# Kernel optimization log

Hardware: AMD Instinct MI355X
Metric: run time of the kernel (lower is better)

Reference implementation:

```python
import jax, jax.numpy as jnp
import numpy as np

N = 100000
E = 1600000


def seg_softmax(alpha, dst, n):
    # numerically stable softmax over variable-size destination segments
    amax = jax.ops.segment_max(alpha, dst, num_segments=n)
    amax = jnp.where(jnp.isfinite(amax), amax, 0.0)
    ex = jnp.exp(alpha - amax[dst])
    denom = jax.ops.segment_sum(ex, dst, num_segments=n)
    return ex / (denom[dst] + 1e-16)


def setup_inputs() -> dict:
    key = jax.random.key(0)
    ks = jax.random.split(key, 24)
    p = lambda k, shape: (jax.random.normal(k, shape, jnp.float32) * 0.1)
    x = jax.random.normal(ks[0], (N, 3), jnp.float32)
    edge_index = jax.random.randint(ks[1], (2, E), 0, N, dtype=jnp.int64)
    return {
        'x': x, 'edge_index': edge_index,
        # GATConv(3,16,heads=4): shared lin (no bias), att_src/att_dst, final bias
        'W1': p(ks[2], (3, 64)), 'att_src1': p(ks[3], (4, 16)), 'att_dst1': p(ks[4], (4, 16)), 'b1': jnp.zeros((64,), jnp.float32),
        # GATv2Conv(64,16,heads=2): lin_l, lin_r (both with bias), att, final bias
        'W2l': p(ks[5], (64, 32)), 'b2l': jnp.zeros((32,), jnp.float32),
        'W2r': p(ks[6], (64, 32)), 'b2r': jnp.zeros((32,), jnp.float32),
        'att2': p(ks[7], (2, 16)), 'b2': jnp.zeros((32,), jnp.float32),
        # TransformerConv(32,7,heads=1): q/k/v lins + skip lin (all with bias)
        'Wq': p(ks[8], (32, 7)), 'bq': jnp.zeros((7,), jnp.float32),
        'Wk': p(ks[9], (32, 7)), 'bk': jnp.zeros((7,), jnp.float32),
        'Wv': p(ks[10], (32, 7)), 'bv': jnp.zeros((7,), jnp.float32),
        'Wskip': p(ks[11], (32, 7)), 'bskip': jnp.zeros((7,), jnp.float32),
    }


def reference(x, edge_index, W1, att_src1, att_dst1, b1, W2l, b2l, W2r, b2r, att2, b2,
              Wq, bq, Wk, bk, Wv, bv, Wskip, bskip):
    n = x.shape[0]
    loop = jnp.arange(n, dtype=edge_index.dtype)
    # edge index with self-loops (GATConv / GATv2Conv default add_self_loops=True)
    src = jnp.concatenate([edge_index[0], loop])
    dst = jnp.concatenate([edge_index[1], loop])

    # ---- layer 1: GATConv(3, 16, heads=4) ----
    h = (x @ W1).reshape(n, 4, 16)                       # [N,H,C]
    a_src = (h * att_src1[None]).sum(-1)                 # [N,H]
    a_dst = (h * att_dst1[None]).sum(-1)
    alpha = jax.nn.leaky_relu(a_src[src] + a_dst[dst], 0.2)  # [E+N,H]
    alpha = seg_softmax(alpha, dst, n)
    out = jax.ops.segment_sum(h[src] * alpha[..., None], dst, num_segments=n)
    x1 = jax.nn.relu(out.reshape(n, 64) + b1)

    # ---- layer 2: GATv2Conv(64, 16, heads=2) ----
    hl = (x1 @ W2l + b2l).reshape(n, 2, 16)
    hr = (x1 @ W2r + b2r).reshape(n, 2, 16)
    e = jax.nn.leaky_relu(hl[src] + hr[dst], 0.2)        # [E+N,H,C]
    alpha = (e * att2[None]).sum(-1)                     # [E+N,H]
    alpha = seg_softmax(alpha, dst, n)
    out = jax.ops.segment_sum(hl[src] * alpha[..., None], dst, num_segments=n)
    x2 = out.reshape(n, 32) + b2

    # ---- layer 3: TransformerConv(32, 7, heads=1); no self-loops by default ----
    s, d = edge_index[0], edge_index[1]
    q = x2 @ Wq + bq                                     # [N,7] (H=1,C=7)
    k = x2 @ Wk + bk
    v = x2 @ Wv + bv
    scale = 1.0 / jnp.sqrt(jnp.float32(7.0))
    alpha = (q[d] * k[s]).sum(-1) * scale                # [E]
    alpha = seg_softmax(alpha, d, n)
    out = jax.ops.segment_sum(v[s] * alpha[:, None], d, num_segments=n)
    x3 = out + (x2 @ Wskip + bskip)                      # root_weight skip connection
    return x3
```

## Files before the change

kernel.cpp:

```cpp
#include <hip/hip_runtime.h>
#include <hip/hip_bf16.h>

typedef __hip_bfloat16 bf16;

static __device__ __forceinline__ float us2f(unsigned short u) {
    union { unsigned int i; float f; } c; c.i = ((unsigned int)u) << 16; return c.f;
}
static __device__ __forceinline__ unsigned short f2us(float f) {
    union { float f; unsigned int i; } c; c.f = f;
    unsigned int r = c.i + 0x7FFF + ((c.i >> 16) & 1);
    return (unsigned short)(r >> 16);
}

static __device__ __forceinline__ int probe_isf32(const unsigned short* xr, int* sflag) {
    int tid = threadIdx.x;
    if (tid < 64) {
        int bad = 0;
        for (int i = tid; i < 1024; i += 64) {
            int ex = (xr[2 * i] >> 7) & 0xFF;
            if (ex < 110 || ex > 135) bad++;
        }
#pragma unroll
        for (int m = 32; m >= 1; m >>= 1) bad += __shfl_xor(bad, m);
        if (tid == 0) *sflag = (bad > 256) ? 1 : 0;
    }
    __syncthreads();
    return *sflag;
}

static __device__ __forceinline__ int ld_edge(const int* er, size_t i, int idx64) {
    return idx64 ? er[2 * i] : er[i];
}


struct CvtArgs { const void* p[19]; int sz[19]; };

static __device__ __forceinline__ float cvt_elem(const void* p, int off, int isf32) {
    return isf32 ? ((const float*)p)[off] : __bfloat162float(((const bf16*)p)[off]);
}

__global__ __launch_bounds__(256) void k_convert(CvtArgs a, float* __restrict__ dst, int total,
                                                 int nbconv, float* __restrict__ Wcat,
                                                 float* __restrict__ bcat, int* __restrict__ bcur) {
    __shared__ int sflag;
    int isf32 = probe_isf32((const unsigned short*)a.p[0], &sflag);
    int tid = threadIdx.x;
    if ((int)blockIdx.x == nbconv) {
#pragma unroll
        for (int t4 = 0; t4 < 4; ++t4) {
            int idx = t4 * 256 + tid;
            int c = idx & 31, g = c >> 3, cc = c & 7, kk = idx >> 5;
            const void* Wg = (g == 0) ? a.p[11] : (g == 1) ? a.p[17] : (g == 2) ? a.p[13] : a.p[15];
            Wcat[idx] = (cc < 7) ? cvt_elem(Wg, kk * 7 + cc, isf32) : 0.f;
        }
        if (tid < 32) {
            int g = tid >> 3, cc = tid & 7;
            const void* Bg = (g == 0) ? a.p[12] : (g == 1) ? a.p[18] : (g == 2) ? a.p[14] : a.p[16];
            bcat[tid] = (cc < 7) ? cvt_elem(Bg, cc, isf32) : 0.f;
        }
        bcur[tid] = 0;
        return;
    }
    int t = blockIdx.x * 256 + tid;
    if (t >= total) return;
    int base = 0, seg = -1, off = 0;
#pragma unroll
    for (int i = 0; i < 19; i++) {
        if (seg < 0 && t < base + a.sz[i]) { seg = i; off = t - base; }
        base += a.sz[i];
    }
    dst[t] = cvt_elem(a.p[seg], off, isf32);
}


__global__ __launch_bounds__(1024) void k_bscatter(const int* __restrict__ er,
                                                   int* __restrict__ bcur, int* __restrict__ bkt,
                                                   int E, int NB, int C) {
    __shared__ int cnt[256];
    __shared__ int res[256];
    __shared__ int sflag;
    int tid = threadIdx.x;
    if (tid < 64) {
        int lim = (E < 1024) ? E : 1024;
        int nz = 0;
        for (int i = tid; i < lim; i += 64) if (er[2 * i + 1] != 0) nz++;
#pragma unroll
        for (int m = 32; m >= 1; m >>= 1) nz += __shfl_xor(nz, m);
        if (tid == 0) sflag = (nz < ((E < 1024 ? E : 1024) >> 1)) ? 1 : 0;
    }
    if (tid < 256) cnt[tid] = 0;
    __syncthreads();
    int idx64 = sflag;
    int base = blockIdx.x * 4096 + tid;
    int pk[4], bv[4];
    bool val[4];
#pragma unroll
    for (int k = 0; k < 4; ++k) {
        int e = base + k * 1024;
        val[k] = (e < E);
        if (val[k]) {
            int s = ld_edge(er, (size_t)e, idx64);
            int d = ld_edge(er, (size_t)E + e, idx64);
            bv[k] = d >> 10;
            pk[k] = (s << 10) | (d & 1023);
            atomicAdd(&cnt[bv[k]], 1);
        }
    }
    __syncthreads();
    if (tid < NB) {
        int c = cnt[tid];
        res[tid] = c ? atomicAdd(&bcur[tid], c) : 0;
        cnt[tid] = 0;
    }
    __syncthreads();
#pragma unroll
    for (int k = 0; k < 4; ++k) {
        if (val[k]) {
            int r = res[bv[k]] + atomicAdd(&cnt[bv[k]], 1);
            if (r < C) bkt[(size_t)bv[k] * C + r] = pk[k];
        }
    }
}

__global__ __launch_bounds__(1024) void k_bbuild(const int* __restrict__ bkt, const int* __restrict__ bcur,
                                                 int2* __restrict__ off2, int* __restrict__ csr, int N, int C) {
    __shared__ int sm[1024];
    int b = blockIdx.x, tid = threadIdx.x;
    size_t base = (size_t)b * C;
    int m = bcur[b]; if (m > C) m = C;
    sm[tid] = 0;
    __syncthreads();
    const int* bp = bkt + base;
    for (int i = tid; i < m; i += 1024) atomicAdd(&sm[bp[i] & 1023], 1);
    __syncthreads();
    int v = sm[tid];
    for (int d = 1; d < 1024; d <<= 1) {
        int t = (tid >= d) ? sm[tid - d] : 0;
        __syncthreads();
        sm[tid] += t;
        __syncthreads();
    }
    int excl = sm[tid] - v;
    int node = (b << 10) + tid;
    if (node < N) off2[node] = make_int2((int)base + excl, (int)base + excl + v);
    __syncthreads();
    sm[tid] = excl;
    __syncthreads();
    for (int i = tid; i < m; i += 1024) {
        int p = bp[i];
        int r = atomicAdd(&sm[p & 1023], 1);
        csr[base + r] = p >> 10;
    }
}


__global__ __launch_bounds__(256) void k_l1_transform(const float* __restrict__ x, const float* __restrict__ W1,
                                                      const float* __restrict__ att_s, const float* __restrict__ att_d,
                                                      float4* __restrict__ x4, float* __restrict__ as1,
                                                      float* __restrict__ ad1, int N) {
    int tid = threadIdx.x;
    int node = blockIdx.x * 4 + (tid >> 6);
    if (node >= N) return;
    int lane = tid & 63;
    float x0 = x[node * 3 + 0];
    float x1 = x[node * 3 + 1];
    float x2 = x[node * 3 + 2];
    float h = x0 * W1[lane] + x1 * W1[64 + lane] + x2 * W1[128 + lane];
    if (lane == 0) x4[node] = make_float4(x0, x1, x2, 0.f);
    float ts = h * att_s[lane];
    float td = h * att_d[lane];
    for (int m = 8; m >= 1; m >>= 1) { ts += __shfl_xor(ts, m); td += __shfl_xor(td, m); }
    if ((lane & 15) == 0) {
        as1[node * 4 + (lane >> 4)] = ts;
        ad1[node * 4 + (lane >> 4)] = td;
    }
}

__global__ __launch_bounds__(256) void k_l1_agg(const float4* __restrict__ x4, const float4* __restrict__ as4,
                                                const float4* __restrict__ ad4p, const int2* __restrict__ off2,
                                                const int* __restrict__ csr, const float* __restrict__ W1,
                                                const float* __restrict__ b1,
                                                float* __restrict__ x1, int N) {
    int tid = threadIdx.x;
    int node = blockIdx.x * 16 + (tid >> 4);
    if (node >= N) return;
    int sl = tid & 15;
    int lane = tid & 63;
    int lb = lane & 48;

    float4 ad = ad4p[node];
    int2 ee = off2[node];
    int e0 = ee.x, e1 = ee.y;

    float v[16];
#pragma unroll
    for (int i = 0; i < 16; ++i) v[i] = 0.f;

    for (int jj = e0 + sl; jj < e1; jj += 16) {
        int s = csr[jj];
        float4 a = as4[s];
        float4 xv = x4[s];
        float z0 = a.x + ad.x, z1 = a.y + ad.y, z2 = a.z + ad.z, z3 = a.w + ad.w;
        z0 = (z0 > 0.f) ? z0 : 0.2f * z0;
        z1 = (z1 > 0.f) ? z1 : 0.2f * z1;
        z2 = (z2 > 0.f) ? z2 : 0.2f * z2;
        z3 = (z3 > 0.f) ? z3 : 0.2f * z3;
        float w0 = __expf(z0), w1 = __expf(z1), w2 = __expf(z2), w3 = __expf(z3);
        v[0] += w0 * xv.x; v[1] += w0 * xv.y; v[2]  += w0 * xv.z; v[3]  += w0;
        v[4] += w1 * xv.x; v[5] += w1 * xv.y; v[6]  += w1 * xv.z; v[7]  += w1;
        v[8] += w2 * xv.x; v[9] += w2 * xv.y; v[10] += w2 * xv.z; v[11] += w2;
        v[12] += w3 * xv.x; v[13] += w3 * xv.y; v[14] += w3 * xv.z; v[15] += w3;
    }

#pragma unroll
    for (int d = 8; d >= 1; d >>= 1) {
#pragma unroll
        for (int i = 0; i < 16; ++i) {
            if (i < d) {
                float a = v[i], b = v[i + d];
                float send = (sl & d) ? a : b;
                float recv = __shfl_xor(send, d);
                v[i] = ((sl & d) ? b : a) + recv;
            }
        }
    }
    float r = v[0];

    float agx[4], agy[4], agz[4], dn[4];
#pragma unroll
    for (int h = 0; h < 4; ++h) {
        agx[h] = __shfl(r, lb + 4 * h + 0);
        agy[h] = __shfl(r, lb + 4 * h + 1);
        agz[h] = __shfl(r, lb + 4 * h + 2);
        dn[h]  = __shfl(r, lb + 4 * h + 3);
    }

    {
        float4 a = as4[node];
        float4 xv = x4[node];
        float z0 = a.x + ad.x, z1 = a.y + ad.y, z2 = a.z + ad.z, z3 = a.w + ad.w;
        z0 = (z0 > 0.f) ? z0 : 0.2f * z0;
        z1 = (z1 > 0.f) ? z1 : 0.2f * z1;
        z2 = (z2 > 0.f) ? z2 : 0.2f * z2;
        z3 = (z3 > 0.f) ? z3 : 0.2f * z3;
        float w0 = __expf(z0), w1 = __expf(z1), w2 = __expf(z2), w3 = __expf(z3);
        agx[0] += w0 * xv.x; agy[0] += w0 * xv.y; agz[0] += w0 * xv.z; dn[0] += w0;
        agx[1] += w1 * xv.x; agy[1] += w1 * xv.y; agz[1] += w1 * xv.z; dn[1] += w1;
        agx[2] += w2 * xv.x; agy[2] += w2 * xv.y; agz[2] += w2 * xv.z; dn[2] += w2;
        agx[3] += w3 * xv.x; agy[3] += w3 * xv.y; agz[3] += w3 * xv.z; dn[3] += w3;
    }

#pragma unroll
    for (int h = 0; h < 4; ++h) {
        int j = h * 16 + sl;
        float inv = 1.f / (dn[h] + 1e-16f);
        float o = (agx[h] * W1[j] + agy[h] * W1[64 + j] + agz[h] * W1[128 + j]) * inv + b1[j];
        x1[(size_t)node * 64 + j] = (o > 0.f) ? o : 0.f;
    }
}


__global__ __launch_bounds__(256) void k_l2_transform(const float* __restrict__ x1,
                                                      const float* __restrict__ W2l, const float* __restrict__ b2l,
                                                      const float* __restrict__ W2r, const float* __restrict__ b2r,
                                                      unsigned short* __restrict__ hlb, float* __restrict__ hr, int N) {
    __shared__ float xs[64 * 68];
    int t = threadIdx.x;
    int node0 = blockIdx.x * 64;
    int nrem = N - node0; if (nrem > 64) nrem = 64;
    const float4* xg = (const float4*)x1;
#pragma unroll
    for (int it = 0; it < 4; ++it) {
        int id = it * 256 + t;
        int row = id >> 4, c4 = id & 15;
        float4 v = make_float4(0.f, 0.f, 0.f, 0.f);
        if (row < nrem) v = xg[(size_t)(node0 + row) * 16 + c4];
        *(float4*)&xs[row * 68 + c4 * 4] = v;
    }
    __syncthreads();
    int nt = t >> 4;
    int jt = t & 15;
    int jq = jt & 7;
    int jc = jq * 4;
    const float4* W4 = (const float4*)((jt < 8) ? W2l : W2r);
    const float4* B4 = (const float4*)((jt < 8) ? b2l : b2r);
    float4 bb = B4[jq];
    float4 acc[4];
#pragma unroll
    for (int i = 0; i < 4; ++i) acc[i] = bb;
#pragma unroll 2
    for (int k4 = 0; k4 < 16; ++k4) {
        float4 w0 = W4[(k4 * 4 + 0) * 8 + jq];
        float4 w1 = W4[(k4 * 4 + 1) * 8 + jq];
        float4 w2 = W4[(k4 * 4 + 2) * 8 + jq];
        float4 w3 = W4[(k4 * 4 + 3) * 8 + jq];
#pragma unroll
        for (int i = 0; i < 4; ++i) {
            float4 xv = *(const float4*)&xs[(nt + i * 16) * 68 + k4 * 4];
            acc[i].x += xv.x * w0.x + xv.y * w1.x + xv.z * w2.x + xv.w * w3.x;
            acc[i].y += xv.x * w0.y + xv.y * w1.y + xv.z * w2.y + xv.w * w3.y;
            acc[i].z += xv.x * w0.z + xv.y * w1.z + xv.z * w2.z + xv.w * w3.z;
            acc[i].w += xv.x * w0.w + xv.y * w1.w + xv.z * w2.w + xv.w * w3.w;
        }
    }
#pragma unroll
    for (int i = 0; i < 4; ++i) {
        int row = nt + i * 16;
        if (row < nrem) {
            size_t node = node0 + row;
            if (jt < 8) {
                uint2 p;
                p.x = (unsigned)f2us(acc[i].x) | ((unsigned)f2us(acc[i].y) << 16);
                p.y = (unsigned)f2us(acc[i].z) | ((unsigned)f2us(acc[i].w) << 16);
                *(uint2*)&hlb[node * 32 + jc] = p;
            } else {
                *(float4*)&hr[node * 32 + jc] = acc[i];
            }
        }
    }
}

__global__ __launch_bounds__(256) void k_l2_agg(const unsigned short* __restrict__ hlb, const float* __restrict__ hr,
                                                const float* __restrict__ att2, const float* __restrict__ b2,
                                                const int2* __restrict__ off2, const int* __restrict__ csr,
                                                float* __restrict__ x2, int N) {
    int tid = threadIdx.x;
    int node = blockIdx.x * 16 + (tid >> 4);
    if (node >= N) return;
    int sl = tid & 15;

    float hrd[32];
    {
        const float4* hr4 = (const float4*)(hr + (size_t)node * 32);
#pragma unroll
        for (int q = 0; q < 8; ++q) {
            float4 v = hr4[q];
            hrd[4 * q + 0] = v.x; hrd[4 * q + 1] = v.y;
            hrd[4 * q + 2] = v.z; hrd[4 * q + 3] = v.w;
        }
    }

    float accA[16], accB[16];
#pragma unroll
    for (int i = 0; i < 16; ++i) { accA[i] = 0.f; accB[i] = 0.f; }
    float den0 = 0.f, den1 = 0.f;

    int2 ee = off2[node];
    int e0 = ee.x, e1 = ee.y;
    for (int jj = e0 + sl; jj < e1; jj += 16) {
        int s = csr[jj];
        const uint4* hp = (const uint4*)(hlb + (size_t)s * 32);
        uint4 u0 = hp[0], u1 = hp[1], u2 = hp[2], u3 = hp[3];
        unsigned int uu[16] = {u0.x, u0.y, u0.z, u0.w, u1.x, u1.y, u1.z, u1.w,
                               u2.x, u2.y, u2.z, u2.w, u3.x, u3.y, u3.z, u3.w};
        float t0 = 0.f, t1 = 0.f;
#pragma unroll
        for (int q = 0; q < 8; ++q) {
            float lo = __uint_as_float(uu[q] << 16);
            float hi = __uint_as_float(uu[q] & 0xFFFF0000u);
            float el = lo + hrd[2 * q];     el = fmaxf(el, 0.2f * el);
            float eh = hi + hrd[2 * q + 1]; eh = fmaxf(eh, 0.2f * eh);
            t0 += att2[2 * q] * el + att2[2 * q + 1] * eh;
        }
#pragma unroll
        for (int q = 8; q < 16; ++q) {
            float lo = __uint_as_float(uu[q] << 16);
            float hi = __uint_as_float(uu[q] & 0xFFFF0000u);
            float el = lo + hrd[2 * q];     el = fmaxf(el, 0.2f * el);
            float eh = hi + hrd[2 * q + 1]; eh = fmaxf(eh, 0.2f * eh);
            t1 += att2[2 * q] * el + att2[2 * q + 1] * eh;
        }
        float w0 = __expf(t0), w1 = __expf(t1);
        den0 += w0; den1 += w1;
#pragma unroll
        for (int q = 0; q < 8; ++q) {
            accA[2 * q]     += w0 * __uint_as_float(uu[q] << 16);
            accA[2 * q + 1] += w0 * __uint_as_float(uu[q] & 0xFFFF0000u);
        }
#pragma unroll
        for (int q = 8; q < 16; ++q) {
            accB[2 * (q - 8)]     += w1 * __uint_as_float(uu[q] << 16);
            accB[2 * (q - 8) + 1] += w1 * __uint_as_float(uu[q] & 0xFFFF0000u);
        }
    }

#pragma unroll
    for (int d = 8; d >= 1; d >>= 1) {
#pragma unroll
        for (int i = 0; i < 16; ++i) {
            if (i < d) {
                { float a = accA[i], b = accA[i + d];
                  float send = (sl & d) ? a : b;
                  float recv = __shfl_xor(send, d);
                  accA[i] = ((sl & d) ? b : a) + recv; }
                { float a = accB[i], b = accB[i + d];
                  float send = (sl & d) ? a : b;
                  float recv = __shfl_xor(send, d);
                  accB[i] = ((sl & d) ? b : a) + recv; }
            }
        }
        den0 += __shfl_xor(den0, d);
        den1 += __shfl_xor(den1, d);
    }
    float sumA = accA[0];
    float sumB = accB[0];

    float hr0 = hr[(size_t)node * 32 + sl];
    float hr1 = hr[(size_t)node * 32 + 16 + sl];
    float hl0 = us2f(hlb[(size_t)node * 32 + sl]);
    float hl1 = us2f(hlb[(size_t)node * 32 + 16 + sl]);
    float ea = hl0 + hr0; ea = fmaxf(ea, 0.2f * ea);
    float eb = hl1 + hr1; eb = fmaxf(eb, 0.2f * eb);
    float p0 = att2[sl] * ea;
    float p1 = att2[16 + sl] * eb;
    p0 += __shfl_xor(p0, 1); p0 += __shfl_xor(p0, 2); p0 += __shfl_xor(p0, 4); p0 += __shfl_xor(p0, 8);
    p1 += __shfl_xor(p1, 1); p1 += __shfl_xor(p1, 2); p1 += __shfl_xor(p1, 4); p1 += __shfl_xor(p1, 8);
    float w0 = __expf(p0), w1 = __expf(p1);
    sumA += w0 * hl0; den0 += w0;
    sumB += w1 * hl1; den1 += w1;

    x2[(size_t)node * 32 + sl]      = sumA / (den0 + 1e-16f) + b2[sl];
    x2[(size_t)node * 32 + 16 + sl] = sumB / (den1 + 1e-16f) + b2[16 + sl];
}


__global__ __launch_bounds__(256) void k_l3_transform(const float* __restrict__ x2,
                                                      const float4* __restrict__ Wc4, const float4* __restrict__ bc4,
                                                      float* __restrict__ QS, unsigned short* __restrict__ KVb, int N) {
    __shared__ float xs[128 * 36];
    int t = threadIdx.x;
    int node0 = blockIdx.x * 128;
    int nrem = N - node0; if (nrem > 128) nrem = 128;
    const float4* xg = (const float4*)x2;
#pragma unroll
    for (int it = 0; it < 4; ++it) {
        int id = it * 256 + t;
        int row = id >> 3, c4 = id & 7;
        float4 v = make_float4(0.f, 0.f, 0.f, 0.f);
        if (row < nrem) v = xg[(size_t)(node0 + row) * 8 + c4];
        *(float4*)&xs[row * 36 + c4 * 4] = v;
    }
    __syncthreads();
    int nt = t >> 3;
    int jt = t & 7;
    float4 bb = bc4[jt];
    float4 acc[4];
#pragma unroll
    for (int i = 0; i < 4; ++i) acc[i] = bb;
#pragma unroll 2
    for (int k4 = 0; k4 < 8; ++k4) {
        float4 w0 = Wc4[(k4 * 4 + 0) * 8 + jt];
        float4 w1 = Wc4[(k4 * 4 + 1) * 8 + jt];
        float4 w2 = Wc4[(k4 * 4 + 2) * 8 + jt];
        float4 w3 = Wc4[(k4 * 4 + 3) * 8 + jt];
#pragma unroll
        for (int i = 0; i < 4; ++i) {
            float4 xv = *(const float4*)&xs[(nt + i * 32) * 36 + k4 * 4];
            acc[i].x += xv.x * w0.x + xv.y * w1.x + xv.z * w2.x + xv.w * w3.x;
            acc[i].y += xv.x * w0.y + xv.y * w1.y + xv.z * w2.y + xv.w * w3.y;
            acc[i].z += xv.x * w0.z + xv.y * w1.z + xv.z * w2.z + xv.w * w3.z;
            acc[i].w += xv.x * w0.w + xv.y * w1.w + xv.z * w2.w + xv.w * w3.w;
        }
    }
#pragma unroll
    for (int i = 0; i < 4; ++i) {
        int row = nt + i * 32;
        if (row < nrem) {
            size_t node = node0 + row;
            if (jt < 4) {
                *(float4*)(QS + node * 16 + jt * 4) = acc[i];
            } else {
                uint2 p;
                p.x = (unsigned)f2us(acc[i].x) | ((unsigned)f2us(acc[i].y) << 16);
                p.y = (unsigned)f2us(acc[i].z) | ((unsigned)f2us(acc[i].w) << 16);
                *(uint2*)&KVb[node * 16 + (size_t)(jt - 4) * 4] = p;
            }
        }
    }
}

__global__ __launch_bounds__(256) void k_l3_agg(const float* __restrict__ QS, const unsigned short* __restrict__ KVb,
                                                const int2* __restrict__ off2, const int* __restrict__ csr,
                                                float* __restrict__ out, int N) {
    int tid = threadIdx.x;
    int node = blockIdx.x * 32 + (tid >> 3);
    if (node >= N) return;
    int sl = tid & 7;
    int lane = tid & 63;
    const float scale = 0.3779644730092272f;
    const float4* q4 = (const float4*)(QS + (size_t)node * 16);
    float4 qa = q4[0], qb = q4[1];
    qa.x *= scale; qa.y *= scale; qa.z *= scale; qa.w *= scale;
    qb.x *= scale; qb.y *= scale; qb.z *= scale; qb.w = 0.f;

    float v[8];
#pragma unroll
    for (int i = 0; i < 8; ++i) v[i] = 0.f;

    int2 ee = off2[node];
    int e0 = ee.x, e1 = ee.y;
    for (int jj = e0 + sl; jj < e1; jj += 8) {
        int s = csr[jj];
        const uint4* kp = (const uint4*)(KVb + (size_t)s * 16);
        uint4 uk = kp[0], uv = kp[1];
        float k0 = __uint_as_float(uk.x << 16),        k1 = __uint_as_float(uk.x & 0xFFFF0000u);
        float k2 = __uint_as_float(uk.y << 16),        k3 = __uint_as_float(uk.y & 0xFFFF0000u);
        float k4 = __uint_as_float(uk.z << 16),        k5 = __uint_as_float(uk.z & 0xFFFF0000u);
        float k6 = __uint_as_float(uk.w << 16);
        float t = qa.x * k0 + qa.y * k1 + qa.z * k2 + qa.w * k3
                + qb.x * k4 + qb.y * k5 + qb.z * k6;
        float w = __expf(t);
        v[0] += w * __uint_as_float(uv.x << 16);
        v[1] += w * __uint_as_float(uv.x & 0xFFFF0000u);
        v[2] += w * __uint_as_float(uv.y << 16);
        v[3] += w * __uint_as_float(uv.y & 0xFFFF0000u);
        v[4] += w * __uint_as_float(uv.z << 16);
        v[5] += w * __uint_as_float(uv.z & 0xFFFF0000u);
        v[6] += w * __uint_as_float(uv.w << 16);
        v[7] += w;
    }
#pragma unroll
    for (int d = 4; d >= 1; d >>= 1) {
#pragma unroll
        for (int i = 0; i < 8; ++i) {
            if (i < d) {
                float a = v[i], b = v[i + d];
                float send = (sl & d) ? a : b;
                float recv = __shfl_xor(send, d);
                v[i] = ((sl & d) ? b : a) + recv;
            }
        }
    }
    float r = v[0];
    float den = __shfl(r, (lane & 56) + 7);
    if (sl < 7) out[(size_t)node * 7 + sl] = r / (den + 1e-16f)
                                             + QS[(size_t)node * 16 + 8 + sl];
}


extern "C" void kernel_launch(void* const* d_in, const int* in_sizes, int n_in,
                              void* d_out, int out_size, void* d_ws, size_t ws_size,
                              hipStream_t stream) {
    const int* ei = (const int*)d_in[1];
    float* out = (float*)d_out;

    int N = in_sizes[0] / 3;
    int E = in_sizes[1] / 2;
    int NB = (N + 1023) >> 10;
    int C = (E + NB - 1) / NB + 4096;

    char* ws = (char*)d_ws;
    size_t o = 0;
    auto take = [&](size_t bytes) -> char* {
        char* p = ws + o;
        o = (o + bytes + 255) & ~(size_t)255;
        return p;
    };
    int total_f = 0;
    for (int i = 0; i < 20; ++i) if (i != 1) total_f += in_sizes[i];
    float* canon   = (float*)take((size_t)total_f * 4);
    float* Wcat    = (float*)take(32 * 32 * 4);
    float* bcat    = (float*)take(32 * 4);
    int2*  off2    = (int2*)take((size_t)N * 8);
    int*   bcur    = (int*)take(256 * 4);
    int*   csr     = (int*)take((size_t)NB * C * 4);
    float* bufA    = (float*)take((size_t)N * 64 * 4);
    float* as1     = (float*)take((size_t)N * 4 * 4);
    float* ad1     = (float*)take((size_t)N * 4 * 4);
    float* bufB    = (float*)take((size_t)N * 64 * 4);
    (void)ws_size; (void)n_in; (void)out_size;

    CvtArgs ca;
    const float* cp[20];
    {
        int off_ = 0, k = 0;
        for (int i = 0; i < 20; ++i) {
            if (i == 1) { cp[i] = nullptr; continue; }
            ca.p[k] = d_in[i];
            ca.sz[k] = in_sizes[i];
            cp[i] = canon + off_;
            off_ += in_sizes[i];
            ++k;
        }
    }

    int nbconv = (total_f + 255) / 256;
    k_convert<<<nbconv + 1, 256, 0, stream>>>(ca, canon, total_f, nbconv, Wcat, bcat, bcur);

    int* bkt = (int*)bufB;
    int gb = (E + 4095) / 4096;
    k_bscatter<<<gb, 1024, 0, stream>>>(ei, bcur, bkt, E, NB, C);
    k_bbuild<<<NB, 1024, 0, stream>>>(bkt, bcur, off2, csr, N, C);

    float4* x4 = (float4*)bufA;
    k_l1_transform<<<(N + 3) / 4, 256, 0, stream>>>(cp[0], cp[2], cp[3], cp[4], x4, as1, ad1, N);
    float* x1 = bufB;
    k_l1_agg<<<(N + 15) / 16, 256, 0, stream>>>(x4, (const float4*)as1, (const float4*)ad1,
                                                off2, csr, cp[2], cp[5], x1, N);

    unsigned short* hlb = (unsigned short*)bufA;
    float* hr = bufA + (size_t)N * 16;
    k_l2_transform<<<(N + 63) / 64, 256, 0, stream>>>(x1, cp[6], cp[7], cp[8], cp[9], hlb, hr, N);
    float* x2 = bufB;
    k_l2_agg<<<(N + 15) / 16, 256, 0, stream>>>(hlb, hr, cp[10], cp[11], off2, csr, x2, N);

    float* QS = bufA;
    unsigned short* KVb = (unsigned short*)(bufA + (size_t)N * 16);
    k_l3_transform<<<(N + 127) / 128, 256, 0, stream>>>(x2, (const float4*)Wcat, (const float4*)bcat,
                                                        QS, KVb, N);
    k_l3_agg<<<(N + 31) / 32, 256, 0, stream>>>(QS, KVb, off2, csr, out, N);
}
```

Baseline: 272.5 us.

## Fuse layer-3 QKV/skip projection into layer-2 aggregation epilogue

The layer-2 aggregation kernel now multiplies its per-node 32-wide output directly by the concatenated layer-3 weight matrix. It reduces the partial products across the 16 lanes with a shuffle transpose-reduce and writes Q/skip in fp32 and K/V in bf16. This removes the separate layer-3 transform kernel, one launch, and the x2 write/read round trip through global memory. In exchange each lane holds a 32-float register array and runs extra shuffles, which may raise register pressure in the aggregation kernel. Outputs go to bufB so they do not overwrite hl/hr in bufA while they are still being read.

```diff
diff --git a/kernel.cpp b/kernel.cpp
--- a/kernel.cpp
+++ b/kernel.cpp
@@ -323,7 +323,8 @@
 __global__ __launch_bounds__(256) void k_l2_agg(const unsigned short* __restrict__ hlb, const float* __restrict__ hr,
                                                 const float* __restrict__ att2, const float* __restrict__ b2,
                                                 const int2* __restrict__ off2, const int* __restrict__ csr,
-                                                float* __restrict__ x2, int N) {
+                                                const float4* __restrict__ Wc4, const float* __restrict__ bcat,
+                                                float* __restrict__ QS, unsigned short* __restrict__ KVb, int N) {
     int tid = threadIdx.x;
     int node = blockIdx.x * 16 + (tid >> 4);
     if (node >= N) return;
@@ -405,7 +406,8 @@
     float sumA = accA[0];
     float sumB = accB[0];
 
-    float hr0 = hr[(size_t)node * 32 + sl];
+    float hr0 = hrd[0];
+    hr0 = hr[(size_t)node * 32 + sl];
     float hr1 = hr[(size_t)node * 32 + 16 + sl];
     float hl0 = us2f(hlb[(size_t)node * 32 + sl]);
     float hl1 = us2f(hlb[(size_t)node * 32 + 16 + sl]);
@@ -419,65 +421,44 @@
     sumA += w0 * hl0; den0 += w0;
     sumB += w1 * hl1; den1 += w1;
 
-    x2[(size_t)node * 32 + sl]      = sumA / (den0 + 1e-16f) + b2[sl];
-    x2[(size_t)node * 32 + 16 + sl] = sumB / (den1 + 1e-16f) + b2[16 + sl];
-}
-
-
-__global__ __launch_bounds__(256) void k_l3_transform(const float* __restrict__ x2,
-                                                      const float4* __restrict__ Wc4, const float4* __restrict__ bc4,
-                                                      float* __restrict__ QS, unsigned short* __restrict__ KVb, int N) {
-    __shared__ float xs[128 * 36];
-    int t = threadIdx.x;
-    int node0 = blockIdx.x * 128;
-    int nrem = N - node0; if (nrem > 128) nrem = 128;
-    const float4* xg = (const float4*)x2;
-#pragma unroll
-    for (int it = 0; it < 4; ++it) {
-        int id = it * 256 + t;
-        int row = id >> 3, c4 = id & 7;
-        float4 v = make_float4(0.f, 0.f, 0.f, 0.f);
-        if (row < nrem) v = xg[(size_t)(node0 + row) * 8 + c4];
-        *(float4*)&xs[row * 36 + c4 * 4] = v;
-    }
-    __syncthreads();
-    int nt = t >> 3;
-    int jt = t & 7;
-    float4 bb = bc4[jt];
-    float4 acc[4];
-#pragma unroll
-    for (int i = 0; i < 4; ++i) acc[i] = bb;
-#pragma unroll 2
-    for (int k4 = 0; k4 < 8; ++k4) {
-        float4 w0 = Wc4[(k4 * 4 + 0) * 8 + jt];
-        float4 w1 = Wc4[(k4 * 4 + 1) * 8 + jt];
-        float4 w2 = Wc4[(k4 * 4 + 2) * 8 + jt];
-        float4 w3 = Wc4[(k4 * 4 + 3) * 8 + jt];
-#pragma unroll
-        for (int i = 0; i < 4; ++i) {
-            float4 xv = *(const float4*)&xs[(nt + i * 32) * 36 + k4 * 4];
-            acc[i].x += xv.x * w0.x + xv.y * w1.x + xv.z * w2.x + xv.w * w3.x;
-            acc[i].y += xv.x * w0.y + xv.y * w1.y + xv.z * w2.y + xv.w * w3.y;
-            acc[i].z += xv.x * w0.z + xv.y * w1.z + xv.z * w2.z + xv.w * w3.z;
-            acc[i].w += xv.x * w0.w + xv.y * w1.w + xv.z * w2.w + xv.w * w3.w;
-        }
-    }
-#pragma unroll
-    for (int i = 0; i < 4; ++i) {
-        int row = nt + i * 32;
-        if (row < nrem) {
-            size_t node = node0 + row;
-            if (jt < 4) {
-                *(float4*)(QS + node * 16 + jt * 4) = acc[i];
-            } else {
-                uint2 p;
-                p.x = (unsigned)f2us(acc[i].x) | ((unsigned)f2us(acc[i].y) << 16);
-                p.y = (unsigned)f2us(acc[i].z) | ((unsigned)f2us(acc[i].w) << 16);
-                *(uint2*)&KVb[node * 16 + (size_t)(jt - 4) * 4] = p;
+    float xa = sumA / (den0 + 1e-16f) + b2[sl];
+    float xb = sumB / (den1 + 1e-16f) + b2[16 + sl];
+
+    float v2[32];
+    {
+        const float4* ra = Wc4 + sl * 8;
+        const float4* rb = Wc4 + (16 + sl) * 8;
+#pragma unroll
+        for (int q = 0; q < 8; ++q) {
+            float4 wa = ra[q], wb = rb[q];
+            v2[4 * q + 0] = xa * wa.x + xb * wb.x;
+            v2[4 * q + 1] = xa * wa.y + xb * wb.y;
+            v2[4 * q + 2] = xa * wa.z + xb * wb.z;
+            v2[4 * q + 3] = xa * wa.w + xb * wb.w;
+        }
+    }
+#pragma unroll
+    for (int d = 8; d >= 1; d >>= 1) {
+#pragma unroll
+        for (int i = 0; i < 32; ++i) {
+            if (i < 2 * d) {
+                float a = v2[i], b = v2[i + 2 * d];
+                float send = (sl & d) ? a : b;
+                float recv = __shfl_xor(send, d);
+                v2[i] = ((sl & d) ? b : a) + recv;
             }
         }
     }
-}
+    float o0 = v2[0] + bcat[2 * sl];
+    float o1 = v2[1] + bcat[2 * sl + 1];
+    if (sl < 8) {
+        *(float2*)&QS[(size_t)node * 16 + 2 * sl] = make_float2(o0, o1);
+    } else {
+        unsigned int p = (unsigned)f2us(o0) | ((unsigned)f2us(o1) << 16);
+        *(unsigned int*)&KVb[(size_t)node * 16 + (2 * sl - 16)] = p;
+    }
+}
+
 
 __global__ __launch_bounds__(256) void k_l3_agg(const float* __restrict__ QS, const unsigned short* __restrict__ KVb,
                                                 const int2* __restrict__ off2, const int* __restrict__ csr,
@@ -601,12 +582,11 @@
     unsigned short* hlb = (unsigned short*)bufA;
     float* hr = bufA + (size_t)N * 16;
     k_l2_transform<<<(N + 63) / 64, 256, 0, stream>>>(x1, cp[6], cp[7], cp[8], cp[9], hlb, hr, N);
-    float* x2 = bufB;
-    k_l2_agg<<<(N + 15) / 16, 256, 0, stream>>>(hlb, hr, cp[10], cp[11], off2, csr, x2, N);
-
-    float* QS = bufA;
-    unsigned short* KVb = (unsigned short*)(bufA + (size_t)N * 16);
-    k_l3_transform<<<(N + 127) / 128, 256, 0, stream>>>(x2, (const float4*)Wcat, (const float4*)bcat,
-                                                        QS, KVb, N);
+
+    float* QS = bufB;
+    unsigned short* KVb = (unsigned short*)(bufB + (size_t)N * 16);
+    k_l2_agg<<<(N + 15) / 16, 256, 0, stream>>>(hlb, hr, cp[10], cp[11], off2, csr,
+                                                (const float4*)Wcat, bcat, QS, KVb, N);
+
     k_l3_agg<<<(N + 31) / 32, 256, 0, stream>>>(QS, KVb, off2, csr, out, N);
 }
```

Result: slower. 296.2 us (+8.7%).
